# Performance work log

Measured on AMD Instinct MI355X. Metric: run time of the kernel, lower is better.

Reference implementation:

```python
import jax, jax.numpy as jnp
import numpy as np

N_NODES = 100000
N_EDGES = 800000
IN_FEAT = 128
HID = 128
OUT = 2


def setup_inputs() -> dict:
    key = jax.random.key(0)
    ks = jax.random.split(key, 8)
    h = jax.random.normal(ks[0], (N_NODES, IN_FEAT), dtype=jnp.float32)
    src = jax.random.randint(ks[1], (N_EDGES,), 0, N_NODES, dtype=jnp.int64)
    dst = jax.random.randint(ks[2], (N_EDGES,), 0, N_NODES, dtype=jnp.int64)
    # Linear weights stored as (fan_in, fan_out); scaled like torch's default init
    W1 = jax.random.normal(ks[3], (2 * IN_FEAT, HID), dtype=jnp.float32) / np.sqrt(2 * IN_FEAT)
    b1 = jnp.zeros((HID,), dtype=jnp.float32)
    W2 = jax.random.normal(ks[4], (HID, HID), dtype=jnp.float32) / np.sqrt(HID)
    b2 = jnp.zeros((HID,), dtype=jnp.float32)
    W3 = jax.random.normal(ks[5], (HID, OUT), dtype=jnp.float32) / np.sqrt(HID)
    b3 = jnp.zeros((OUT,), dtype=jnp.float32)
    return {"h": h, "src": src, "dst": dst,
            "W1": W1, "b1": b1, "W2": W2, "b2": b2, "W3": W3, "b3": b3}


def reference(h, src, dst, W1, b1, W2, b2, W3, b3):
    # Per-edge gather of endpoint features, concat, 3-layer MLP with ReLU
    h_u = h[src]                       # [E, F]
    h_v = h[dst]                       # [E, F]
    x = jnp.concatenate([h_u, h_v], axis=1)   # [E, 2F]
    x = jax.nn.relu(x @ W1 + b1)       # [E, HID]
    x = jax.nn.relu(x @ W2 + b2)       # [E, HID]
    score = x @ W3 + b3                # [E, OUT]
    return score
```

## Files before the change

### kernel.cpp

```cpp
#include <hip/hip_runtime.h>
#include <hip/hip_fp16.h>


typedef _Float16 half8 __attribute__((ext_vector_type(8)));
typedef _Float16 half4_t __attribute__((ext_vector_type(4)));
typedef float    f32x4 __attribute__((ext_vector_type(4)));

#define MFMA16(a, b, c) __builtin_amdgcn_mfma_f32_16x16x32_f16((a), (b), (c), 0, 0, 0)

#define N_NODES_C 100000
#define N_EDGES_C 800000

#define W1PF_OFF  0
#define W1QF_OFF  32768
#define W2F_OFF_N 65536
#define W3F_OFF_N 98304
#define P16_OFF   131072
#define TBL_HALVES (N_NODES_C * 128)
#define Q16_OFF   (P16_OFF + TBL_HALVES * 2)
#define WS_NEED_NEW ((size_t)Q16_OFF + (size_t)TBL_HALVES * 2)

#define ET 32
#define NT_E (N_EDGES_C / ET)
#define GRID_E 1024
#define NT_N ((N_NODES_C + 63) / 64)


__global__ void pack_w_new(const float* __restrict__ W1, const float* __restrict__ W2,
                           const float* __restrict__ W3, char* __restrict__ wsb) {
    int i = blockIdx.x * blockDim.x + threadIdx.x;
    _Float16* w1pf = (_Float16*)(wsb + W1PF_OFF);
    _Float16* w1qf = (_Float16*)(wsb + W1QF_OFF);
    _Float16* w2f  = (_Float16*)(wsb + W2F_OFF_N);
    _Float16* w3f  = (_Float16*)(wsb + W3F_OFF_N);
    if (i < 16384) {
        int j = i & 7, lane = (i >> 3) & 63, kk = (i >> 9) & 3, cm = i >> 11;
        int g = lane >> 4, rr = lane & 15;
        int k = 32 * kk + 8 * g + j, n = 16 * cm + rr;
        w1pf[i] = (_Float16)W1[k * 128 + n];
        w1qf[i] = (_Float16)W1[(k + 128) * 128 + n];
        w2f[i]  = (_Float16)W2[k * 128 + n];
    }
    if (i < 2048) {
        int j = i & 7, lane = (i >> 3) & 63, t = i >> 9;
        int g = lane >> 4, rr = lane & 15;
        int k = 32 * t + 4 * g + (j & 3) + 16 * (j >> 2);
        w3f[i] = (rr < 2) ? (_Float16)W3[k * 2 + rr] : (_Float16)0.0f;
    }
}

__global__ __launch_bounds__(512, 4) void pq_kernel(const float* __restrict__ h,
                                                    const float* __restrict__ b1,
                                                    char* __restrict__ wsb) {
    __shared__ float4 Htile[64 * 32];
    const int tid = threadIdx.x;
    const int w = tid >> 6, l = tid & 63, g = l >> 4, rr = l & 15;
    const int t = w >> 2, cmq = w & 3;
    const half8* wf = (const half8*)(wsb + (t ? W1QF_OFF : W1PF_OFF));
    half8 W1F[2][4];
#pragma unroll
    for (int cm = 0; cm < 2; ++cm)
#pragma unroll
        for (int kk = 0; kk < 4; ++kk)
            W1F[cm][kk] = wf[((2 * cmq + cm) * 4 + kk) * 64 + l];
    f32x4 b1v[2] = {{0.f, 0.f, 0.f, 0.f}, {0.f, 0.f, 0.f, 0.f}};
    if (t == 1) {
#pragma unroll
        for (int cm = 0; cm < 2; ++cm)
            b1v[cm] = *(const f32x4*)(b1 + 16 * (2 * cmq + cm) + 4 * g);
    }
    _Float16* tbl = (_Float16*)(wsb + (t ? Q16_OFF : P16_OFF));

    const int tile = blockIdx.x;
    const int slot = l & 31, rhalf = l >> 5;
    float4 sv[4];
    int rows[4];
#pragma unroll
    for (int i = 0; i < 4; ++i) {
        int row = 8 * w + 2 * i + rhalf;
        rows[i] = row;
        int node = tile * 64 + row;
        if (node > N_NODES_C - 1) node = N_NODES_C - 1;
        sv[i] = *(const float4*)(h + (size_t)node * 128 + slot * 4);
    }
#pragma unroll
    for (int i = 0; i < 4; ++i)
        Htile[rows[i] * 32 + (slot ^ (rows[i] & 15))] = sv[i];
    __syncthreads();

    f32x4 acc[2][4];
#pragma unroll
    for (int cm = 0; cm < 2; ++cm)
#pragma unroll
        for (int ce = 0; ce < 4; ++ce) acc[cm][ce] = f32x4{0.f, 0.f, 0.f, 0.f};
#pragma unroll
    for (int kk = 0; kk < 4; ++kk) {
#pragma unroll
        for (int ce = 0; ce < 4; ++ce) {
            int row = 16 * ce + rr;
            int s0 = kk * 8 + 2 * g;
            float4 fa = Htile[row * 32 + (s0 ^ rr)];
            float4 fb = Htile[row * 32 + ((s0 + 1) ^ rr)];
            half8 b;
            b[0] = (_Float16)fa.x; b[1] = (_Float16)fa.y;
            b[2] = (_Float16)fa.z; b[3] = (_Float16)fa.w;
            b[4] = (_Float16)fb.x; b[5] = (_Float16)fb.y;
            b[6] = (_Float16)fb.z; b[7] = (_Float16)fb.w;
            acc[0][ce] = MFMA16(W1F[0][kk], b, acc[0][ce]);
            acc[1][ce] = MFMA16(W1F[1][kk], b, acc[1][ce]);
        }
    }
#pragma unroll
    for (int cm = 0; cm < 2; ++cm)
#pragma unroll
        for (int ce = 0; ce < 4; ++ce) {
            int node = tile * 64 + 16 * ce + rr;
            if (node < N_NODES_C) {
                f32x4 v = acc[cm][ce] + b1v[cm];
                half4_t o;
                o[0] = (_Float16)v[0]; o[1] = (_Float16)v[1];
                o[2] = (_Float16)v[2]; o[3] = (_Float16)v[3];
                *(half4_t*)(tbl + (size_t)node * 128 + 16 * (2 * cmq + cm) + 4 * g) = o;
            }
        }
}

__global__ __launch_bounds__(128, 3) void edge_kernel(
    const int* __restrict__ src, const int* __restrict__ dst,
    const float* __restrict__ b2, const float* __restrict__ b3,
    const char* __restrict__ wsb, float* __restrict__ out) {
    __shared__ half8 W2lds[2048];
    __shared__ float2 part[2][2][16];
    const int tid = threadIdx.x;
    const int w = tid >> 6, l = tid & 63, g = l >> 4, rr = l & 15;
    const half8* w2fg = (const half8*)(wsb + W2F_OFF_N);
    const half8* w3f = (const half8*)(wsb + W3F_OFF_N);
    const half8* P16 = (const half8*)(wsb + P16_OFF);
    const half8* Q16 = (const half8*)(wsb + Q16_OFF);

#pragma unroll
    for (int i = 0; i < 16; ++i) W2lds[i * 128 + tid] = w2fg[i * 128 + tid];

    half8 W3F[2];
    W3F[0] = w3f[(2 * w) * 64 + l];
    W3F[1] = w3f[(2 * w + 1) * 64 + l];

    half4_t b2h[4];
#pragma unroll
    for (int cm = 0; cm < 4; ++cm) {
        f32x4 bv = *(const f32x4*)(b2 + 16 * (4 * w + cm) + 4 * g);
        b2h[cm][0] = (_Float16)bv[0]; b2h[cm][1] = (_Float16)bv[1];
        b2h[cm][2] = (_Float16)bv[2]; b2h[cm][3] = (_Float16)bv[3];
    }
    const float b30 = b3[0], b31 = b3[1];

    int tile = blockIdx.x;
    int sc0 = src[tile * ET + rr],      sc1 = src[tile * ET + 16 + rr];
    int dc0 = dst[tile * ET + rr],      dc1 = dst[tile * ET + 16 + rr];
    int par = 0;
    __syncthreads();

    for (; tile < NT_E; tile += GRID_E) {
        int ntile = tile + GRID_E; if (ntile >= NT_E) ntile = NT_E - 1;
        const half8* pr0 = P16 + (size_t)sc0 * 16 + g;
        const half8* pr1 = P16 + (size_t)sc1 * 16 + g;
        const half8* qr0 = Q16 + (size_t)dc0 * 16 + g;
        const half8* qr1 = Q16 + (size_t)dc1 * 16 + g;

        half8 P0[4], P1[4], Q0[4], Q1[4];
#pragma unroll
        for (int kk = 0; kk < 4; ++kk) {
            P0[kk] = pr0[4 * kk];
            Q0[kk] = qr0[4 * kk];
            P1[kk] = pr1[4 * kk];
            Q1[kk] = qr1[4 * kk];
        }
        int sn0 = src[ntile * ET + rr], sn1 = src[ntile * ET + 16 + rr];
        int dn0 = dst[ntile * ET + rr], dn1 = dst[ntile * ET + 16 + rr];

        f32x4 acc[4][2];
#pragma unroll
        for (int cm = 0; cm < 4; ++cm) {
            acc[cm][0] = f32x4{0.f, 0.f, 0.f, 0.f};
            acc[cm][1] = f32x4{0.f, 0.f, 0.f, 0.f};
        }
        const half8 hz = {0, 0, 0, 0, 0, 0, 0, 0};
#pragma unroll
        for (int kk = 0; kk < 4; ++kk) {
            half8 bq0 = __builtin_elementwise_max(P0[kk] + Q0[kk], hz);
            half8 bq1 = __builtin_elementwise_max(P1[kk] + Q1[kk], hz);
#pragma unroll
            for (int cm = 0; cm < 4; ++cm) {
                half8 wfr = W2lds[((4 * w + cm) * 4 + kk) * 64 + l];
                acc[cm][0] = MFMA16(wfr, bq0, acc[cm][0]);
                acc[cm][1] = MFMA16(wfr, bq1, acc[cm][1]);
            }
        }

        f32x4 D3[2] = {{0.f, 0.f, 0.f, 0.f}, {0.f, 0.f, 0.f, 0.f}};
#pragma unroll
        for (int tl = 0; tl < 2; ++tl)
#pragma unroll
            for (int ce = 0; ce < 2; ++ce) {
                half8 bf;
#pragma unroll
                for (int j = 0; j < 8; ++j) {
                    const int cm = 2 * tl + (j >> 2), r = j & 3;
                    float v = acc[cm][ce][r] + (float)b2h[cm][r];
                    v = v > 0.f ? v : 0.f;
                    bf[j] = (_Float16)v;
                }
                D3[ce] = MFMA16(W3F[tl], bf, D3[ce]);
            }
        if (w == 1 && l < 16) {
            part[par][0][rr] = make_float2(D3[0][0], D3[0][1]);
            part[par][1][rr] = make_float2(D3[1][0], D3[1][1]);
        }
        __syncthreads();
        if (w == 0 && l < 16) {
#pragma unroll
            for (int ce = 0; ce < 2; ++ce) {
                float2 pp = part[par][ce][rr];
                float2 ov;
                ov.x = D3[ce][0] + pp.x + b30;
                ov.y = D3[ce][1] + pp.y + b31;
                *(float2*)(out + (size_t)(tile * ET + 16 * ce + rr) * 2) = ov;
            }
        }
        par ^= 1;
        sc0 = sn0; sc1 = sn1; dc0 = dn0; dc1 = dn1;
    }
}


#define NT_O   12500
#define GRID_O 512
#define OW1_OFF 0
#define OW2_OFF 65536
#define OW3_OFF 98304

__global__ void pack_w_old(const float* __restrict__ W1, const float* __restrict__ W2,
                           const float* __restrict__ W3, char* __restrict__ wsb) {
    int i = blockIdx.x * blockDim.x + threadIdx.x;
    _Float16* w1f = (_Float16*)(wsb + OW1_OFF);
    _Float16* w2f = (_Float16*)(wsb + OW2_OFF);
    _Float16* w3f = (_Float16*)(wsb + OW3_OFF);
    if (i < 32768) {
        int j = i & 7, lx = (i >> 3) & 63, kk = (i >> 9) & 7, t = i >> 12;
        int k = 32 * kk + 8 * (lx >> 4) + j, n = 16 * t + (lx & 15);
        w1f[i] = (_Float16)W1[k * 128 + n];
    }
    if (i < 16384) {
        int j = i & 7, lx = (i >> 3) & 63, kk = (i >> 9) & 3, t = i >> 11;
        int k = 32 * kk + 8 * (lx >> 4) + j, n = 16 * t + (lx & 15);
        w2f[i] = (_Float16)W2[k * 128 + n];
    }
    if (i < 2048) {
        int j = i & 7, lx = (i >> 3) & 63, kk = i >> 9;
        int k = 32 * kk + 8 * (lx >> 4) + j, n = lx & 15;
        w3f[i] = (n < 2) ? (_Float16)W3[k * 2 + n] : (_Float16)0.0f;
    }
}

__device__ inline half8 ldfrag_f32(const float* __restrict__ h, int idx, int kk, int g) {
    const float4* p = (const float4*)(h + (size_t)idx * 128 + (kk & 3) * 32 + g * 8);
    float4 a = p[0], b = p[1];
    half8 o;
    o[0] = (_Float16)a.x; o[1] = (_Float16)a.y; o[2] = (_Float16)a.z; o[3] = (_Float16)a.w;
    o[4] = (_Float16)b.x; o[5] = (_Float16)b.y; o[6] = (_Float16)b.z; o[7] = (_Float16)b.w;
    return o;
}

__global__ __launch_bounds__(256, 2) void edge_mlp_old(
    const float* __restrict__ h, const int* __restrict__ src, const int* __restrict__ dst,
    const float* __restrict__ b1, const float* __restrict__ b2, const float* __restrict__ b3,
    const char* __restrict__ wsb, float* __restrict__ out) {
    __shared__ half8 Xp [32 * 64];
    __shared__ half8 Y1p[16 * 64];
    __shared__ half8 Y2p[16 * 64];
    const int tid = threadIdx.x;
    const int w = tid >> 6, l = tid & 63;
    const int g = l >> 4, rr = l & 15;
    const int ghalf = rr >> 3, j7 = rr & 7;
    half8 W1F[2][8], W2F[2][4], W3F[4];
    {
        const half8* p1 = (const half8*)(wsb + OW1_OFF);
        const half8* p2 = (const half8*)(wsb + OW2_OFF);
        const half8* p3 = (const half8*)(wsb + OW3_OFF);
#pragma unroll
        for (int nt = 0; nt < 2; ++nt)
#pragma unroll
            for (int kk = 0; kk < 8; ++kk) W1F[nt][kk] = p1[((w * 2 + nt) * 8 + kk) * 64 + l];
#pragma unroll
        for (int nt = 0; nt < 2; ++nt)
#pragma unroll
            for (int kk = 0; kk < 4; ++kk) W2F[nt][kk] = p2[((w * 2 + nt) * 4 + kk) * 64 + l];
#pragma unroll
        for (int kk = 0; kk < 4; ++kk) W3F[kk] = p3[kk * 64 + l];
    }
    float b1r[2], b2r[2];
    b1r[0] = b1[w * 32 + rr];      b1r[1] = b1[w * 32 + 16 + rr];
    b2r[0] = b2[w * 32 + rr];      b2r[1] = b2[w * 32 + 16 + rr];
    const float b3r = (rr < 2) ? b3[rr] : 0.0f;
    _Float16* y1h = (_Float16*)Y1p;
    _Float16* y2h = (_Float16*)Y2p;
    int   idxn[8];
    half8 xt[8];
    int tile = blockIdx.x;
#pragma unroll
    for (int i = 0; i < 8; i++) {
        int bidx = w * 8 + i, kk = bidx >> 2;
        int e = ((i & 3) << 4) + rr;
        int id = (kk < 4 ? src : dst)[tile * 64 + e];
        xt[i] = ldfrag_f32(h, id, kk, g);
    }
#pragma unroll
    for (int i = 0; i < 8; i++) Xp[(w * 8 + i) * 64 + l] = xt[i];
    {
        int t1 = tile + GRID_O; if (t1 >= NT_O) t1 = NT_O - 1;
#pragma unroll
        for (int i = 0; i < 8; i++) {
            int bidx = w * 8 + i, kk = bidx >> 2;
            int e = ((i & 3) << 4) + rr;
            idxn[i] = (kk < 4 ? src : dst)[t1 * 64 + e];
        }
    }
    __syncthreads();
    for (; tile < NT_O; tile += GRID_O) {
        f32x4 acc1[4][2];
#pragma unroll
        for (int mt = 0; mt < 4; ++mt) {
            acc1[mt][0] = f32x4{0.f, 0.f, 0.f, 0.f};
            acc1[mt][1] = f32x4{0.f, 0.f, 0.f, 0.f};
        }
#pragma unroll
        for (int kk = 0; kk < 8; ++kk) {
            half8 a[4];
#pragma unroll
            for (int mt = 0; mt < 4; ++mt) a[mt] = Xp[(kk * 4 + mt) * 64 + l];
#pragma unroll
            for (int mt = 0; mt < 4; ++mt) {
                acc1[mt][0] = MFMA16(a[mt], W1F[0][kk], acc1[mt][0]);
                acc1[mt][1] = MFMA16(a[mt], W1F[1][kk], acc1[mt][1]);
            }
        }
#pragma unroll
        for (int i = 0; i < 8; i++) {
            int kk = (w * 8 + i) >> 2;
            xt[i] = ldfrag_f32(h, idxn[i], kk, g);
        }
        {
            int t2 = tile + 2 * GRID_O; if (t2 >= NT_O) t2 = NT_O - 1;
#pragma unroll
            for (int i = 0; i < 8; i++) {
                int bidx = w * 8 + i, kk = bidx >> 2;
                int e = ((i & 3) << 4) + rr;
                idxn[i] = (kk < 4 ? src : dst)[t2 * 64 + e];
            }
        }
#pragma unroll
        for (int mt = 0; mt < 4; ++mt)
#pragma unroll
            for (int nt = 0; nt < 2; ++nt) {
                float bb = b1r[nt];
#pragma unroll
                for (int r = 0; r < 4; ++r) {
                    float v = acc1[mt][nt][r] + bb;
                    v = v > 0.f ? v : 0.f;
                    y1h[(((w * 4 + mt) * 64 + 16 * (2 * nt + ghalf) + 4 * g + r) << 3) + j7] =
                        (_Float16)v;
                }
            }
        __syncthreads();
        f32x4 acc2[4][2];
#pragma unroll
        for (int mt = 0; mt < 4; ++mt) {
            acc2[mt][0] = f32x4{0.f, 0.f, 0.f, 0.f};
            acc2[mt][1] = f32x4{0.f, 0.f, 0.f, 0.f};
        }
#pragma unroll
        for (int kk = 0; kk < 4; ++kk) {
            half8 a[4];
#pragma unroll
            for (int mt = 0; mt < 4; ++mt) a[mt] = Y1p[(kk * 4 + mt) * 64 + l];
#pragma unroll
            for (int mt = 0; mt < 4; ++mt) {
                acc2[mt][0] = MFMA16(a[mt], W2F[0][kk], acc2[mt][0]);
                acc2[mt][1] = MFMA16(a[mt], W2F[1][kk], acc2[mt][1]);
            }
        }
#pragma unroll
        for (int mt = 0; mt < 4; ++mt)
#pragma unroll
            for (int nt = 0; nt < 2; ++nt) {
                float bb = b2r[nt];
#pragma unroll
                for (int r = 0; r < 4; ++r) {
                    float v = acc2[mt][nt][r] + bb;
                    v = v > 0.f ? v : 0.f;
                    y2h[(((w * 4 + mt) * 64 + 16 * (2 * nt + ghalf) + 4 * g + r) << 3) + j7] =
                        (_Float16)v;
                }
            }
        __syncthreads();
        f32x4 acc3 = {0.f, 0.f, 0.f, 0.f};
#pragma unroll
        for (int kk = 0; kk < 4; ++kk) {
            half8 a = Y2p[(kk * 4 + w) * 64 + l];
            acc3 = MFMA16(a, W3F[kk], acc3);
        }
        if (rr < 2) {
#pragma unroll
            for (int r = 0; r < 4; ++r) {
                int m = w * 16 + 4 * g + r;
                out[(tile * 64 + m) * 2 + rr] = acc3[r] + b3r;
            }
        }
#pragma unroll
        for (int i = 0; i < 8; i++) Xp[(w * 8 + i) * 64 + l] = xt[i];
        __syncthreads();
    }
}


extern "C" void kernel_launch(void* const* d_in, const int* in_sizes, int n_in,
                              void* d_out, int out_size, void* d_ws, size_t ws_size,
                              hipStream_t stream) {
    const float* h   = (const float*)d_in[0];
    const int*   src = (const int*)d_in[1];
    const int*   dst = (const int*)d_in[2];
    const float* W1  = (const float*)d_in[3];
    const float* b1  = (const float*)d_in[4];
    const float* W2  = (const float*)d_in[5];
    const float* b2  = (const float*)d_in[6];
    const float* W3  = (const float*)d_in[7];
    const float* b3  = (const float*)d_in[8];
    char*  wsb = (char*)d_ws;
    float* out = (float*)d_out;
    (void)in_sizes; (void)n_in; (void)out_size;

    if (ws_size >= WS_NEED_NEW) {
        pack_w_new<<<64, 256, 0, stream>>>(W1, W2, W3, wsb);
        pq_kernel<<<NT_N, 512, 0, stream>>>(h, b1, wsb);
        edge_kernel<<<GRID_E, 128, 0, stream>>>(src, dst, b2, b3, wsb, out);
    } else {
        pack_w_old<<<128, 256, 0, stream>>>(W1, W2, W3, wsb);
        edge_mlp_old<<<GRID_O, 256, 0, stream>>>(h, src, dst, b1, b2, b3, wsb, out);
    }
}
```

Baseline: 218.7 us.

## Double-buffer edge feature gathers across tiles in edge kernel

Restructures the edge loop into a two-stage software pipeline: the gathered P/Q rows for the next tile are issued before computing the current tile, using ping-pong register buffers, and the indices are prefetched two tiles ahead. A sched_barrier stops the compiler from sinking the loads past the compute. This is meant to hide gather latency behind the MFMA work. It doubles the gather registers held per thread, so launch bounds drop from 3 to 2 blocks per SIMD, which lowers occupancy.

```diff
diff --git a/kernel.cpp b/kernel.cpp
--- a/kernel.cpp
+++ b/kernel.cpp
@@ -125,7 +125,81 @@
         }
 }
 
-__global__ __launch_bounds__(128, 3) void edge_kernel(
+
+#define IDXLOAD(T, s0, s1, d0, d1)                            \
+    {                                                          \
+        int tt = (T); if (tt >= NT_E) tt = NT_E - 1;           \
+        s0 = src[tt * ET + rr];  s1 = src[tt * ET + 16 + rr];  \
+        d0 = dst[tt * ET + rr];  d1 = dst[tt * ET + 16 + rr];  \
+    }
+
+#define LOADSET(SP0, SP1, SQ0, SQ1, s0, s1, d0, d1)            \
+    {                                                          \
+        const half8* pr0 = P16 + (size_t)(s0) * 16 + g;        \
+        const half8* pr1 = P16 + (size_t)(s1) * 16 + g;        \
+        const half8* qr0 = Q16 + (size_t)(d0) * 16 + g;        \
+        const half8* qr1 = Q16 + (size_t)(d1) * 16 + g;        \
+        _Pragma("unroll")                                      \
+        for (int kk = 0; kk < 4; ++kk) {                       \
+            SP0[kk] = pr0[4 * kk];  SQ0[kk] = qr0[4 * kk];     \
+            SP1[kk] = pr1[4 * kk];  SQ1[kk] = qr1[4 * kk];     \
+        }                                                      \
+    }
+
+#define COMPUTE_STORE(SP0, SP1, SQ0, SQ1, TILE)                                 \
+    {                                                                           \
+        f32x4 acc[4][2];                                                        \
+        _Pragma("unroll")                                                       \
+        for (int cm = 0; cm < 4; ++cm) {                                        \
+            acc[cm][0] = f32x4{0.f, 0.f, 0.f, 0.f};                             \
+            acc[cm][1] = f32x4{0.f, 0.f, 0.f, 0.f};                             \
+        }                                                                       \
+        const half8 hz = {0, 0, 0, 0, 0, 0, 0, 0};                              \
+        _Pragma("unroll")                                                       \
+        for (int kk = 0; kk < 4; ++kk) {                                        \
+            half8 bq0 = __builtin_elementwise_max(SP0[kk] + SQ0[kk], hz);       \
+            half8 bq1 = __builtin_elementwise_max(SP1[kk] + SQ1[kk], hz);       \
+            _Pragma("unroll")                                                   \
+            for (int cm = 0; cm < 4; ++cm) {                                    \
+                half8 wfr = W2lds[((4 * w + cm) * 4 + kk) * 64 + l];            \
+                acc[cm][0] = MFMA16(wfr, bq0, acc[cm][0]);                      \
+                acc[cm][1] = MFMA16(wfr, bq1, acc[cm][1]);                      \
+            }                                                                   \
+        }                                                                       \
+        f32x4 D3[2] = {{0.f, 0.f, 0.f, 0.f}, {0.f, 0.f, 0.f, 0.f}};             \
+        _Pragma("unroll")                                                       \
+        for (int tl = 0; tl < 2; ++tl)                                          \
+            _Pragma("unroll")                                                   \
+            for (int ce = 0; ce < 2; ++ce) {                                    \
+                half8 bf;                                                       \
+                _Pragma("unroll")                                               \
+                for (int j = 0; j < 8; ++j) {                                   \
+                    const int cm = 2 * tl + (j >> 2), r = j & 3;                \
+                    float v = acc[cm][ce][r] + (float)b2h[cm][r];               \
+                    v = v > 0.f ? v : 0.f;                                      \
+                    bf[j] = (_Float16)v;                                        \
+                }                                                               \
+                D3[ce] = MFMA16(W3F[tl], bf, D3[ce]);                           \
+            }                                                                   \
+        if (w == 1 && l < 16) {                                                 \
+            part[par][0][rr] = make_float2(D3[0][0], D3[0][1]);                 \
+            part[par][1][rr] = make_float2(D3[1][0], D3[1][1]);                 \
+        }                                                                       \
+        __syncthreads();                                                        \
+        if (w == 0 && l < 16) {                                                 \
+            _Pragma("unroll")                                                   \
+            for (int ce = 0; ce < 2; ++ce) {                                    \
+                float2 pp = part[par][ce][rr];                                  \
+                float2 ov;                                                      \
+                ov.x = D3[ce][0] + pp.x + b30;                                  \
+                ov.y = D3[ce][1] + pp.y + b31;                                  \
+                *(float2*)(out + (size_t)((TILE) * ET + 16 * ce + rr) * 2) = ov;\
+            }                                                                   \
+        }                                                                       \
+        par ^= 1;                                                               \
+    }
+
+__global__ __launch_bounds__(128, 2) void edge_kernel(
     const int* __restrict__ src, const int* __restrict__ dst,
     const float* __restrict__ b2, const float* __restrict__ b3,
     const char* __restrict__ wsb, float* __restrict__ out) {
@@ -153,82 +227,33 @@
         b2h[cm][2] = (_Float16)bv[2]; b2h[cm][3] = (_Float16)bv[3];
     }
     const float b30 = b3[0], b31 = b3[1];
+    int par = 0;
+
+    half8 PA0[4], PA1[4], QA0[4], QA1[4];
+    half8 PB0[4], PB1[4], QB0[4], QB1[4];
+    int ia0, ia1, ja0, ja1;
+    int ib0, ib1, jb0, jb1;
 
     int tile = blockIdx.x;
-    int sc0 = src[tile * ET + rr],      sc1 = src[tile * ET + 16 + rr];
-    int dc0 = dst[tile * ET + rr],      dc1 = dst[tile * ET + 16 + rr];
-    int par = 0;
+    IDXLOAD(tile, ia0, ia1, ja0, ja1);
+    LOADSET(PA0, PA1, QA0, QA1, ia0, ia1, ja0, ja1);
+    IDXLOAD(tile + GRID_E, ib0, ib1, jb0, jb1);
     __syncthreads();
 
-    for (; tile < NT_E; tile += GRID_E) {
-        int ntile = tile + GRID_E; if (ntile >= NT_E) ntile = NT_E - 1;
-        const half8* pr0 = P16 + (size_t)sc0 * 16 + g;
-        const half8* pr1 = P16 + (size_t)sc1 * 16 + g;
-        const half8* qr0 = Q16 + (size_t)dc0 * 16 + g;
-        const half8* qr1 = Q16 + (size_t)dc1 * 16 + g;
-
-        half8 P0[4], P1[4], Q0[4], Q1[4];
-#pragma unroll
-        for (int kk = 0; kk < 4; ++kk) {
-            P0[kk] = pr0[4 * kk];
-            Q0[kk] = qr0[4 * kk];
-            P1[kk] = pr1[4 * kk];
-            Q1[kk] = qr1[4 * kk];
-        }
-        int sn0 = src[ntile * ET + rr], sn1 = src[ntile * ET + 16 + rr];
-        int dn0 = dst[ntile * ET + rr], dn1 = dst[ntile * ET + 16 + rr];
-
-        f32x4 acc[4][2];
-#pragma unroll
-        for (int cm = 0; cm < 4; ++cm) {
-            acc[cm][0] = f32x4{0.f, 0.f, 0.f, 0.f};
-            acc[cm][1] = f32x4{0.f, 0.f, 0.f, 0.f};
-        }
-        const half8 hz = {0, 0, 0, 0, 0, 0, 0, 0};
-#pragma unroll
-        for (int kk = 0; kk < 4; ++kk) {
-            half8 bq0 = __builtin_elementwise_max(P0[kk] + Q0[kk], hz);
-            half8 bq1 = __builtin_elementwise_max(P1[kk] + Q1[kk], hz);
-#pragma unroll
-            for (int cm = 0; cm < 4; ++cm) {
-                half8 wfr = W2lds[((4 * w + cm) * 4 + kk) * 64 + l];
-                acc[cm][0] = MFMA16(wfr, bq0, acc[cm][0]);
-                acc[cm][1] = MFMA16(wfr, bq1, acc[cm][1]);
-            }
-        }
-
-        f32x4 D3[2] = {{0.f, 0.f, 0.f, 0.f}, {0.f, 0.f, 0.f, 0.f}};
-#pragma unroll
-        for (int tl = 0; tl < 2; ++tl)
-#pragma unroll
-            for (int ce = 0; ce < 2; ++ce) {
-                half8 bf;
-#pragma unroll
-                for (int j = 0; j < 8; ++j) {
-                    const int cm = 2 * tl + (j >> 2), r = j & 3;
-                    float v = acc[cm][ce][r] + (float)b2h[cm][r];
-                    v = v > 0.f ? v : 0.f;
-                    bf[j] = (_Float16)v;
-                }
-                D3[ce] = MFMA16(W3F[tl], bf, D3[ce]);
-            }
-        if (w == 1 && l < 16) {
-            part[par][0][rr] = make_float2(D3[0][0], D3[0][1]);
-            part[par][1][rr] = make_float2(D3[1][0], D3[1][1]);
-        }
-        __syncthreads();
-        if (w == 0 && l < 16) {
-#pragma unroll
-            for (int ce = 0; ce < 2; ++ce) {
-                float2 pp = part[par][ce][rr];
-                float2 ov;
-                ov.x = D3[ce][0] + pp.x + b30;
-                ov.y = D3[ce][1] + pp.y + b31;
-                *(float2*)(out + (size_t)(tile * ET + 16 * ce + rr) * 2) = ov;
-            }
-        }
-        par ^= 1;
-        sc0 = sn0; sc1 = sn1; dc0 = dn0; dc1 = dn1;
+    for (;;) {
+        LOADSET(PB0, PB1, QB0, QB1, ib0, ib1, jb0, jb1);
+        __builtin_amdgcn_sched_barrier(0);
+        IDXLOAD(tile + 2 * GRID_E, ia0, ia1, ja0, ja1);
+        COMPUTE_STORE(PA0, PA1, QA0, QA1, tile);
+        tile += GRID_E;
+        if (tile >= NT_E) break;
+
+        LOADSET(PA0, PA1, QA0, QA1, ia0, ia1, ja0, ja1);
+        __builtin_amdgcn_sched_barrier(0);
+        IDXLOAD(tile + 2 * GRID_E, ib0, ib1, jb0, jb1);
+        COMPUTE_STORE(PB0, PB1, QB0, QB1, tile);
+        tile += GRID_E;
+        if (tile >= NT_E) break;
     }
 }
 
```

New measurement: 215.8 us. Within noise of the previous version (-1.4%).
